# Optimization experiments

Measured on AMD Instinct MI355X. Metric: run time of the kernel, lower is better.

## Reference

```python
import jax, jax.numpy as jnp
import numpy as np

NEMBED, EMBED_DIM, HID_DIM, OUT_DIM, NUM_CLASSES = 128, 64, 128, 128, 2
BATCH, TEAM = 2048, 5
N_OPS = 8


def setup_inputs() -> dict:
    key = jax.random.key(0)
    ks = jax.random.split(key, 8)
    w_eq = np.sqrt(2.0 / (EMBED_DIM + HID_DIM + N_OPS))
    return {
        "x": jax.random.randint(ks[0], (BATCH, 2, TEAM), 0, NEMBED, dtype=jnp.int32),
        "embed": jax.random.normal(ks[1], (NEMBED, EMBED_DIM), jnp.float32) * 0.1,
        "coefs1": jax.random.normal(ks[2], (EMBED_DIM, HID_DIM, N_OPS), jnp.float32) * w_eq,
        "bias1": jnp.zeros((HID_DIM,), jnp.float32),
        "wout1": jax.random.normal(ks[3], (HID_DIM, OUT_DIM), jnp.float32) * np.sqrt(1.0 / HID_DIM),
        "bout1": jnp.zeros((OUT_DIM,), jnp.float32),
        "coefs2": jax.random.normal(ks[4], (EMBED_DIM, HID_DIM, N_OPS), jnp.float32) * w_eq,
        "bias2": jnp.zeros((HID_DIM,), jnp.float32),
        "wout2": jax.random.normal(ks[5], (HID_DIM, OUT_DIM), jnp.float32) * np.sqrt(1.0 / HID_DIM),
        "bout2": jnp.zeros((OUT_DIM,), jnp.float32),
        "fcw": jax.random.normal(ks[6], (2 * OUT_DIM, NCLS := NUM_CLASSES and 2 * OUT_DIM and NUM_CLASSES), jnp.float32) * np.sqrt(1.0 / (2 * OUT_DIM)),
        "fcb": jnp.zeros((NUM_CLASSES,), jnp.float32),
    }


def eset_ops_3_to_3(t):
    # t: (N, D, m, m, m). 8 equivariant basis ops: keep-or-(sum&broadcast) each axis.
    # Pooled ops are kept with singleton dims; broadcasting happens after the
    # channel contraction (cheaper, same math as expand-then-contract).
    s1 = t.sum(-3, keepdims=True)
    s2 = t.sum(-2, keepdims=True)
    s3 = t.sum(-1, keepdims=True)
    s12 = t.sum((-3, -2), keepdims=True)
    s13 = t.sum((-3, -1), keepdims=True)
    s23 = t.sum((-2, -1), keepdims=True)
    sall = t.sum((-3, -2, -1), keepdims=True)
    return [t, s1, s2, s3, s12, s13, s23, sall]


def eq3_layer(t, coefs, bias):
    # coefs: (D_in, D_out, 8); output (N, D_out, m, m, m)
    ops = eset_ops_3_to_3(t)
    out = 0.0
    for b, op in enumerate(ops):
        out = out + jnp.einsum('ndijk,ds->nsijk', op, coefs[:, :, b])
    return out + bias[None, :, None, None, None]


def setnet3to3(t, coefs, bias, wout, bout):
    h = jax.nn.relu(eq3_layer(t, coefs, bias))          # (N, H, m, m, m)
    return jnp.einsum('nsijk,so->nijko', h, wout) + bout  # (N, m, m, m, out_dim)


def reference(x, embed, coefs1, bias1, wout1, bout1, coefs2, bias2, wout2, bout2, fcw, fcb):
    e1 = jax.nn.relu(embed[x[:, 0]])  # (N, 5, D)
    e2 = jax.nn.relu(embed[x[:, 1]])
    t1 = jnp.einsum('bid,bjd,bkd->bdijk', e1, e1, e1)  # (N, D, 5, 5, 5)
    t2 = jnp.einsum('bid,bjd,bkd->bdijk', e2, e2, e2)
    o1 = setnet3to3(t1, coefs1, bias1, wout1, bout1)
    o2 = setnet3to3(t2, coefs2, bias2, wout2, bout2)
    t1e = jax.nn.relu(o1.mean(axis=(1, 2, 3)))  # (N, out_dim)
    t2e = jax.nn.relu(o2.mean(axis=(1, 2, 3)))
    z = jnp.concatenate([t1e, t2e], axis=-1)    # dropout_prob=0 / eval mode: no-op
    return z @ fcw + fcb
```

## Files before the change

### kernel.cpp

```cpp
#include <hip/hip_runtime.h>


typedef __attribute__((ext_vector_type(8))) short bf16x8;
typedef __attribute__((ext_vector_type(4))) float f32x4;
typedef __attribute__((ext_vector_type(4))) unsigned u32x4;

#define DEV __device__ __forceinline__
#define MFMA __builtin_amdgcn_mfma_f32_16x16x32_bf16

DEV constexpr int pid2(int a, int b) {
  int x = a < b ? a : b, y = a < b ? b : a;
  return x * (9 - x) / 2 + y;
}
DEV constexpr int tid3(int i, int j, int k) {
  int a = i, b = j, c = k, t;
  if (a > b) { t = a; a = b; b = t; }
  if (b > c) { t = b; b = c; c = t; }
  if (a > b) { t = a; a = b; b = t; }
  return a * (a * a - 18 * a + 107) / 6 + (b - a) * (11 - a - b) / 2 + (c - b);
}
DEV ushort f2bf(float f) {
  unsigned u = __builtin_bit_cast(unsigned, f);
  return (ushort)((u + 0x7FFFu + ((u >> 16) & 1u)) >> 16);
}
DEV unsigned pk2(float a, float b) {
  return (unsigned)f2bf(a) | ((unsigned)f2bf(b) << 16);
}

__global__ __launch_bounds__(256)
void prep_kernel(const float* __restrict__ c1, const float* __restrict__ c2,
                 const float* __restrict__ w1, const float* __restrict__ w2,
                 ushort* __restrict__ ctf, float* __restrict__ wt, int do_wt) {
  const int idx = blockIdx.x * 256 + threadIdx.x;
  if (idx < 131072) {
    const int e = idx & 7, l = (idx >> 3) & 63, nt = (idx >> 9) & 7,
              kt = (idx >> 12) & 1, bank = (idx >> 13) & 7, side = (idx >> 16) & 1;
    const int d = 32 * kt + 8 * (l >> 4) + e;
    const int s = 16 * nt + (l & 15);
    ctf[idx] = f2bf((side ? c2 : c1)[(d * 128 + s) * 8 + bank]);
  } else if (do_wt) {
    const int j = idx - 131072;
    if (j < 65536) {
      const int s = j & 127, o = (j >> 7) & 127, side = j >> 14;
      wt[j] = (side ? w2 : w1)[s * 128 + o] * (1.f / 125.f);
    }
  }
}

__global__ __launch_bounds__(256, 3)
void eq3_wavegemm(const int* __restrict__ x, const float* __restrict__ embed,
                  const float* __restrict__ bias1, const float* __restrict__ bias2,
                  const float* __restrict__ bout1, const float* __restrict__ bout2,
                  const float* __restrict__ wout1, const float* __restrict__ wout2,
                  const float* __restrict__ fcw,
                  const ushort* __restrict__ ctf, const float* __restrict__ wt,
                  float* __restrict__ pbuf, int nunits)
{
  __shared__ ushort FT[80 * 64];
  __shared__ ushort TS[8 * 2184];
  __shared__ float  S2[256];
  __shared__ float  SW[256];
  __shared__ float  fcp[4];

  const int tid = threadIdx.x;
  const int w = tid >> 6, l = tid & 63, grp = l >> 4, lc = l & 15;

  for (int e = tid; e < 24 * 64; e += 256) {
    const int r = e >> 6, d = e & 63;
    const int row = (r < 13) ? 35 + r : ((r == 13) ? 63 : 70 + (r - 14));
    FT[(row * 64 + d) ^ ((row & 7) << 3)] = 0;
  }
  int uprev = -1;

  for (int u = blockIdx.x; u < nunits; u += gridDim.x) {
    const int side = u & 1;

    {
      const int d = tid & 63, q = tid >> 6;
      const int* xn = x + u * 5;
      float v[5];
      #pragma unroll
      for (int i = 0; i < 5; ++i) v[i] = fmaxf(embed[xn[i] * 64 + d], 0.f);
      const float Sv = v[0] + v[1] + v[2] + v[3] + v[4];
      const float Sq = Sv * Sv, Sc = Sq * Sv;
      float p2a[15];
      {
        int c2 = 0;
        #pragma unroll
        for (int a = 0; a < 5; ++a)
          #pragma unroll
          for (int b = a; b < 5; ++b) { p2a[c2] = v[a] * v[b]; ++c2; }
      }
      {
        int c3 = 0;
        #pragma unroll
        for (int a = 0; a < 5; ++a)
          #pragma unroll
          for (int b = a; b < 5; ++b)
            #pragma unroll
            for (int c = b; c < 5; ++c) {
              const int qq = (c3 < 14) ? 0 : ((c3 < 28) ? 1 : 2);
              if (q == qq)
                FT[(c3 * 64 + d) ^ ((c3 & 7) << 3)] = f2bf(p2a[pid2(a, b)] * v[c]);
              ++c3;
            }
      }
      #pragma unroll
      for (int p = 0; p < 15; ++p) {
        const int qq = (p < 7) ? 2 : 3;
        const int row = 48 + p;
        if (q == qq) FT[(row * 64 + d) ^ ((row & 7) << 3)] = f2bf(Sv * p2a[p]);
      }
      if (q == 3) {
        #pragma unroll
        for (int i = 0; i < 5; ++i) {
          const int row = 64 + i;
          FT[(row * 64 + d) ^ ((row & 7) << 3)] = f2bf(Sq * v[i]);
        }
        FT[(69 * 64 + d) ^ ((69 & 7) << 3)] = f2bf(Sc);
      }
    }
    __syncthreads();

    if (uprev >= 0 && tid == 0) {
      pbuf[2 * uprev]     = fcp[0] + fcp[2];
      pbuf[2 * uprev + 1] = fcp[1] + fcp[3];
    }

    {
      const ushort* cbase = ctf + side * 65536;
      #pragma unroll
      for (int sub = 0; sub < 2; ++sub) {
        const int nti = 2 * w + sub;
        auto FR = [&](int t0, int kt) -> bf16x8 {
          const int t = t0 + lc;
          return *(const bf16x8*)(FT + ((t * 64 + 32 * kt + 8 * grp) ^ ((t & 7) << 3)));
        };
        auto CR = [&](int bank, int kt) -> bf16x8 {
          return *(const bf16x8*)(cbase + (((bank * 2 + kt) * 8 + nti) * 64 + l) * 8);
        };
        ushort* tb = TS + nti * 2184 + lc * 136;
        f32x4 a;
        a = {0.f, 0.f, 0.f, 0.f};
        a = MFMA(FR(0, 0), CR(0, 0), a, 0, 0, 0);
        a = MFMA(FR(0, 1), CR(0, 1), a, 0, 0, 0);
        { uint2 t2; t2.x = pk2(a[0], a[1]); t2.y = pk2(a[2], a[3]);
          *reinterpret_cast<uint2*>(tb + 4 * grp) = t2; }
        a = {0.f, 0.f, 0.f, 0.f};
        a = MFMA(FR(16, 0), CR(0, 0), a, 0, 0, 0);
        a = MFMA(FR(16, 1), CR(0, 1), a, 0, 0, 0);
        { uint2 t2; t2.x = pk2(a[0], a[1]); t2.y = pk2(a[2], a[3]);
          *reinterpret_cast<uint2*>(tb + 16 + 4 * grp) = t2; }
        a = {0.f, 0.f, 0.f, 0.f};
        a = MFMA(FR(32, 0), CR(0, 0), a, 0, 0, 0);
        a = MFMA(FR(32, 1), CR(0, 1), a, 0, 0, 0);
        if (grp == 0) {
          *reinterpret_cast<unsigned*>(tb + 32) = pk2(a[0], a[1]);
          tb[34] = f2bf(a[2]);
        }
        {
          const bf16x8 A0 = FR(48, 0), A1 = FR(48, 1);
          #pragma unroll
          for (int bk = 1; bk <= 3; ++bk) {
            const int cb = 48 + 16 * (bk - 1);
            a = {0.f, 0.f, 0.f, 0.f};
            a = MFMA(A0, CR(bk, 0), a, 0, 0, 0);
            a = MFMA(A1, CR(bk, 1), a, 0, 0, 0);
            if (grp < 3) {
              uint2 t2; t2.x = pk2(a[0], a[1]); t2.y = pk2(a[2], a[3]);
              *reinterpret_cast<uint2*>(tb + cb + 4 * grp) = t2;
            } else {
              *reinterpret_cast<unsigned*>(tb + cb + 12) = pk2(a[0], a[1]);
              tb[cb + 14] = f2bf(a[2]);
            }
          }
        }
        {
          const bf16x8 A0 = FR(64, 0), A1 = FR(64, 1);
          #pragma unroll
          for (int bk = 4; bk <= 6; ++bk) {
            const int cb = 96 + 8 * (bk - 4);
            a = {0.f, 0.f, 0.f, 0.f};
            a = MFMA(A0, CR(bk, 0), a, 0, 0, 0);
            a = MFMA(A1, CR(bk, 1), a, 0, 0, 0);
            if (grp == 0) {
              uint2 t2; t2.x = pk2(a[0], a[1]); t2.y = pk2(a[2], a[3]);
              *reinterpret_cast<uint2*>(tb + cb) = t2;
            } else if (grp == 1) {
              tb[cb + 4] = f2bf(a[0]);
            }
          }
          a = {0.f, 0.f, 0.f, 0.f};
          a = MFMA(A0, CR(7, 0), a, 0, 0, 0);
          a = MFMA(A1, CR(7, 1), a, 0, 0, 0);
          if (grp == 1) tb[120] = f2bf(a[1]);
        }
      }
    }
    __syncthreads();

    {
      const int ch = tid & 127, half = tid >> 7;
      const ushort* trow = TS + (ch >> 4) * 2184 + (ch & 15) * 136;
      u32x4 R[16];
      #pragma unroll
      for (int j = 0; j < 16; ++j) R[j] = *(const u32x4*)(trow + 8 * j);
      __builtin_amdgcn_sched_barrier(0);
      auto ext = [&](int c) -> float {
        const unsigned wv = R[c >> 3][(c >> 1) & 3];
        return __builtin_bit_cast(float, (c & 1) ? (wv & 0xFFFF0000u) : (wv << 16));
      };
      const float* bi = side ? bias2 : bias1;
      const float base = ext(120) + bi[ch];
      float hs = 0.f;
      #define CELLK(i, j, k)                                                      \
        hs += fmaxf(pij + ext(96 + (k)) + ext(64 + pid2(i, k)) +                  \
                    ext(48 + pid2(j, k)) + ext(tid3(i, j, k)), 0.f);
      if (half == 0) {
        #pragma unroll
        for (int i = 0; i < 2; ++i) {
          const float pi = base + ext(112 + i);
          #pragma unroll
          for (int j = 0; j < 5; ++j) {
            const float pij = pi + ext(104 + j) + ext(80 + pid2(i, j));
            #pragma unroll
            for (int k = 0; k < 5; ++k) CELLK(i, j, k)
          }
        }
        {
          const float pi = base + ext(112 + 2);
          #pragma unroll
          for (int j = 0; j < 2; ++j) {
            const float pij = pi + ext(104 + j) + ext(80 + pid2(2, j));
            #pragma unroll
            for (int k = 0; k < 5; ++k) CELLK(2, j, k)
          }
          {
            const float pij = pi + ext(104 + 2) + ext(80 + pid2(2, 2));
            #pragma unroll
            for (int k = 0; k < 3; ++k) CELLK(2, 2, k)
          }
        }
      } else {
        {
          const float pi = base + ext(112 + 2);
          {
            const float pij = pi + ext(104 + 2) + ext(80 + pid2(2, 2));
            #pragma unroll
            for (int k = 3; k < 5; ++k) CELLK(2, 2, k)
          }
          #pragma unroll
          for (int j = 3; j < 5; ++j) {
            const float pij = pi + ext(104 + j) + ext(80 + pid2(2, j));
            #pragma unroll
            for (int k = 0; k < 5; ++k) CELLK(2, j, k)
          }
        }
        #pragma unroll
        for (int i = 3; i < 5; ++i) {
          const float pi = base + ext(112 + i);
          #pragma unroll
          for (int j = 0; j < 5; ++j) {
            const float pij = pi + ext(104 + j) + ext(80 + pid2(i, j));
            #pragma unroll
            for (int k = 0; k < 5; ++k) CELLK(i, j, k)
          }
        }
      }
      #undef CELLK
      S2[half * 128 + ch] = hs;
    }
    __syncthreads();

    {
      const int o = tid & 127, h = tid >> 7;
      float r;
      if (wt != nullptr) {
        const f32x4* wv = (const f32x4*)(wt + side * 16384 + o * 128 + h * 64);
        const f32x4* pa = (const f32x4*)(S2 + h * 64);
        const f32x4* pb = (const f32x4*)(S2 + 128 + h * 64);
        float a0 = 0.f, a1 = 0.f, a2 = 0.f, a3 = 0.f;
        #pragma unroll
        for (int q2 = 0; q2 < 16; ++q2) {
          const f32x4 hq = pa[q2] + pb[q2];
          const f32x4 wq = wv[q2];
          a0 = fmaf(hq[0], wq[0], a0);
          a1 = fmaf(hq[1], wq[1], a1);
          a2 = fmaf(hq[2], wq[2], a2);
          a3 = fmaf(hq[3], wq[3], a3);
        }
        r = (a0 + a1) + (a2 + a3);
      } else {
        const float* W = side ? wout2 : wout1;
        float acc = 0.f;
        #pragma unroll 8
        for (int s = 64 * h; s < 64 * h + 64; ++s)
          acc = fmaf((S2[s] + S2[128 + s]) * (1.f / 125.f), W[s * 128 + o], acc);
        r = acc;
      }
      SW[h * 128 + o] = r;
    }
    __syncthreads();

    if (tid < 128) {
      const int o = tid;
      const float* bo = side ? bout2 : bout1;
      const float z = fmaxf(SW[o] + SW[128 + o] + bo[o], 0.f);
      const float* fw = fcw + side * 256;
      float p0 = z * fw[2 * o], p1 = z * fw[2 * o + 1];
      #pragma unroll
      for (int off = 32; off; off >>= 1) {
        p0 += __shfl_down(p0, off);
        p1 += __shfl_down(p1, off);
      }
      if ((tid & 63) == 0) { fcp[(tid >> 6) * 2] = p0; fcp[(tid >> 6) * 2 + 1] = p1; }
    }
    uprev = u;
  }

  if (uprev >= 0) {
    __syncthreads();
    if (tid == 0) {
      pbuf[2 * uprev]     = fcp[0] + fcp[2];
      pbuf[2 * uprev + 1] = fcp[1] + fcp[3];
    }
  }
}

__global__ __launch_bounds__(256)
void fc_final(const float* __restrict__ pbuf, const float* __restrict__ fcb,
              float* __restrict__ out, int nout) {
  const int t = blockIdx.x * 256 + threadIdx.x;
  if (t < nout) {
    const int n = t >> 1, c = t & 1;
    out[t] = pbuf[4 * n + c] + pbuf[4 * n + 2 + c] + fcb[c];
  }
}

extern "C" void kernel_launch(void* const* d_in, const int* in_sizes, int n_in,
                              void* d_out, int out_size, void* d_ws, size_t ws_size,
                              hipStream_t stream) {
  const int*   x      = (const int*)  d_in[0];
  const float* embed  = (const float*)d_in[1];
  const float* coefs1 = (const float*)d_in[2];
  const float* bias1  = (const float*)d_in[3];
  const float* wout1  = (const float*)d_in[4];
  const float* bout1  = (const float*)d_in[5];
  const float* coefs2 = (const float*)d_in[6];
  const float* bias2  = (const float*)d_in[7];
  const float* wout2  = (const float*)d_in[8];
  const float* bout2  = (const float*)d_in[9];
  const float* fcw    = (const float*)d_in[10];
  const float* fcb    = (const float*)d_in[11];
  float* out = (float*)d_out;

  float*  pbuf = (float*)d_ws;
  ushort* ctf  = (ushort*)((char*)d_ws + 32768);
  const int do_wt = (ws_size >= (size_t)(32768 + 262144 + 131072)) ? 1 : 0;
  float*  wt   = do_wt ? (float*)((char*)d_ws + 32768 + 262144) : nullptr;

  const int batch  = in_sizes[0] / 10;
  const int nunits = batch * 2;

  prep_kernel<<<768, 256, 0, stream>>>(coefs1, coefs2, wout1, wout2, ctf, wt, do_wt);
  eq3_wavegemm<<<2048, 256, 0, stream>>>(
      x, embed, bias1, bias2, bout1, bout2, wout1, wout2, fcw, ctf, wt, pbuf, nunits);
  fc_final<<<(nunits + 255) / 256, 256, 0, stream>>>(pbuf, fcb, out, nunits);
}
```

Before: 92.64 us.

## Use 512-thread blocks with 8 waves, one N-tile per wave

Doubles the block to 8 waves so each wave computes a single MFMA N-tile instead of two, and splits the 125-cell ReLU pass and the output projection four ways across channels instead of two. The grid shrinks from 2048 to 512 persistent blocks, each looping over more units. The aim is shorter per-unit critical paths and more parallel work inside each block. The trade-off is fewer blocks, different occupancy limits and the same number of barriers per unit shared across more threads.

```diff
diff --git a/kernel.cpp b/kernel.cpp
--- a/kernel.cpp
+++ b/kernel.cpp
@@ -47,25 +47,25 @@
   }
 }
 
-__global__ __launch_bounds__(256, 3)
-void eq3_wavegemm(const int* __restrict__ x, const float* __restrict__ embed,
-                  const float* __restrict__ bias1, const float* __restrict__ bias2,
-                  const float* __restrict__ bout1, const float* __restrict__ bout2,
-                  const float* __restrict__ wout1, const float* __restrict__ wout2,
-                  const float* __restrict__ fcw,
-                  const ushort* __restrict__ ctf, const float* __restrict__ wt,
-                  float* __restrict__ pbuf, int nunits)
+__global__ __launch_bounds__(512, 4)
+void eq3_w8(const int* __restrict__ x, const float* __restrict__ embed,
+            const float* __restrict__ bias1, const float* __restrict__ bias2,
+            const float* __restrict__ bout1, const float* __restrict__ bout2,
+            const float* __restrict__ wout1, const float* __restrict__ wout2,
+            const float* __restrict__ fcw,
+            const ushort* __restrict__ ctf, const float* __restrict__ wt,
+            float* __restrict__ pbuf, int nunits)
 {
   __shared__ ushort FT[80 * 64];
   __shared__ ushort TS[8 * 2184];
-  __shared__ float  S2[256];
-  __shared__ float  SW[256];
+  __shared__ float  S2[512];
+  __shared__ float  SW[512];
   __shared__ float  fcp[4];
 
   const int tid = threadIdx.x;
   const int w = tid >> 6, l = tid & 63, grp = l >> 4, lc = l & 15;
 
-  for (int e = tid; e < 24 * 64; e += 256) {
+  for (int e = tid; e < 24 * 64; e += 512) {
     const int r = e >> 6, d = e & 63;
     const int row = (r < 13) ? 35 + r : ((r == 13) ? 63 : 70 + (r - 14));
     FT[(row * 64 + d) ^ ((row & 7) << 3)] = 0;
@@ -99,19 +99,18 @@
           for (int b = a; b < 5; ++b)
             #pragma unroll
             for (int c = b; c < 5; ++c) {
-              const int qq = (c3 < 14) ? 0 : ((c3 < 28) ? 1 : 2);
-              if (q == qq)
+              if (q == c3 / 7)
                 FT[(c3 * 64 + d) ^ ((c3 & 7) << 3)] = f2bf(p2a[pid2(a, b)] * v[c]);
               ++c3;
             }
       }
       #pragma unroll
       for (int p = 0; p < 15; ++p) {
-        const int qq = (p < 7) ? 2 : 3;
         const int row = 48 + p;
-        if (q == qq) FT[(row * 64 + d) ^ ((row & 7) << 3)] = f2bf(Sv * p2a[p]);
-      }
-      if (q == 3) {
+        if (q == (35 + p) / 7)
+          FT[(row * 64 + d) ^ ((row & 7) << 3)] = f2bf(Sv * p2a[p]);
+      }
+      if (q == 7) {
         #pragma unroll
         for (int i = 0; i < 5; ++i) {
           const int row = 64 + i;
@@ -129,78 +128,75 @@
 
     {
       const ushort* cbase = ctf + side * 65536;
-      #pragma unroll
-      for (int sub = 0; sub < 2; ++sub) {
-        const int nti = 2 * w + sub;
-        auto FR = [&](int t0, int kt) -> bf16x8 {
-          const int t = t0 + lc;
-          return *(const bf16x8*)(FT + ((t * 64 + 32 * kt + 8 * grp) ^ ((t & 7) << 3)));
-        };
-        auto CR = [&](int bank, int kt) -> bf16x8 {
-          return *(const bf16x8*)(cbase + (((bank * 2 + kt) * 8 + nti) * 64 + l) * 8);
-        };
-        ushort* tb = TS + nti * 2184 + lc * 136;
-        f32x4 a;
-        a = {0.f, 0.f, 0.f, 0.f};
-        a = MFMA(FR(0, 0), CR(0, 0), a, 0, 0, 0);
-        a = MFMA(FR(0, 1), CR(0, 1), a, 0, 0, 0);
-        { uint2 t2; t2.x = pk2(a[0], a[1]); t2.y = pk2(a[2], a[3]);
-          *reinterpret_cast<uint2*>(tb + 4 * grp) = t2; }
-        a = {0.f, 0.f, 0.f, 0.f};
-        a = MFMA(FR(16, 0), CR(0, 0), a, 0, 0, 0);
-        a = MFMA(FR(16, 1), CR(0, 1), a, 0, 0, 0);
-        { uint2 t2; t2.x = pk2(a[0], a[1]); t2.y = pk2(a[2], a[3]);
-          *reinterpret_cast<uint2*>(tb + 16 + 4 * grp) = t2; }
-        a = {0.f, 0.f, 0.f, 0.f};
-        a = MFMA(FR(32, 0), CR(0, 0), a, 0, 0, 0);
-        a = MFMA(FR(32, 1), CR(0, 1), a, 0, 0, 0);
-        if (grp == 0) {
-          *reinterpret_cast<unsigned*>(tb + 32) = pk2(a[0], a[1]);
-          tb[34] = f2bf(a[2]);
-        }
-        {
-          const bf16x8 A0 = FR(48, 0), A1 = FR(48, 1);
-          #pragma unroll
-          for (int bk = 1; bk <= 3; ++bk) {
-            const int cb = 48 + 16 * (bk - 1);
-            a = {0.f, 0.f, 0.f, 0.f};
-            a = MFMA(A0, CR(bk, 0), a, 0, 0, 0);
-            a = MFMA(A1, CR(bk, 1), a, 0, 0, 0);
-            if (grp < 3) {
-              uint2 t2; t2.x = pk2(a[0], a[1]); t2.y = pk2(a[2], a[3]);
-              *reinterpret_cast<uint2*>(tb + cb + 4 * grp) = t2;
-            } else {
-              *reinterpret_cast<unsigned*>(tb + cb + 12) = pk2(a[0], a[1]);
-              tb[cb + 14] = f2bf(a[2]);
-            }
+      const int nti = w;
+      auto FR = [&](int t0, int kt) -> bf16x8 {
+        const int t = t0 + lc;
+        return *(const bf16x8*)(FT + ((t * 64 + 32 * kt + 8 * grp) ^ ((t & 7) << 3)));
+      };
+      auto CR = [&](int bank, int kt) -> bf16x8 {
+        return *(const bf16x8*)(cbase + (((bank * 2 + kt) * 8 + nti) * 64 + l) * 8);
+      };
+      ushort* tb = TS + nti * 2184 + lc * 136;
+      f32x4 a;
+      a = {0.f, 0.f, 0.f, 0.f};
+      a = MFMA(FR(0, 0), CR(0, 0), a, 0, 0, 0);
+      a = MFMA(FR(0, 1), CR(0, 1), a, 0, 0, 0);
+      { uint2 t2; t2.x = pk2(a[0], a[1]); t2.y = pk2(a[2], a[3]);
+        *reinterpret_cast<uint2*>(tb + 4 * grp) = t2; }
+      a = {0.f, 0.f, 0.f, 0.f};
+      a = MFMA(FR(16, 0), CR(0, 0), a, 0, 0, 0);
+      a = MFMA(FR(16, 1), CR(0, 1), a, 0, 0, 0);
+      { uint2 t2; t2.x = pk2(a[0], a[1]); t2.y = pk2(a[2], a[3]);
+        *reinterpret_cast<uint2*>(tb + 16 + 4 * grp) = t2; }
+      a = {0.f, 0.f, 0.f, 0.f};
+      a = MFMA(FR(32, 0), CR(0, 0), a, 0, 0, 0);
+      a = MFMA(FR(32, 1), CR(0, 1), a, 0, 0, 0);
+      if (grp == 0) {
+        *reinterpret_cast<unsigned*>(tb + 32) = pk2(a[0], a[1]);
+        tb[34] = f2bf(a[2]);
+      }
+      {
+        const bf16x8 A0 = FR(48, 0), A1 = FR(48, 1);
+        #pragma unroll
+        for (int bk = 1; bk <= 3; ++bk) {
+          const int cb = 48 + 16 * (bk - 1);
+          a = {0.f, 0.f, 0.f, 0.f};
+          a = MFMA(A0, CR(bk, 0), a, 0, 0, 0);
+          a = MFMA(A1, CR(bk, 1), a, 0, 0, 0);
+          if (grp < 3) {
+            uint2 t2; t2.x = pk2(a[0], a[1]); t2.y = pk2(a[2], a[3]);
+            *reinterpret_cast<uint2*>(tb + cb + 4 * grp) = t2;
+          } else {
+            *reinterpret_cast<unsigned*>(tb + cb + 12) = pk2(a[0], a[1]);
+            tb[cb + 14] = f2bf(a[2]);
           }
         }
-        {
-          const bf16x8 A0 = FR(64, 0), A1 = FR(64, 1);
-          #pragma unroll
-          for (int bk = 4; bk <= 6; ++bk) {
-            const int cb = 96 + 8 * (bk - 4);
-            a = {0.f, 0.f, 0.f, 0.f};
-            a = MFMA(A0, CR(bk, 0), a, 0, 0, 0);
-            a = MFMA(A1, CR(bk, 1), a, 0, 0, 0);
-            if (grp == 0) {
-              uint2 t2; t2.x = pk2(a[0], a[1]); t2.y = pk2(a[2], a[3]);
-              *reinterpret_cast<uint2*>(tb + cb) = t2;
-            } else if (grp == 1) {
-              tb[cb + 4] = f2bf(a[0]);
-            }
+      }
+      {
+        const bf16x8 A0 = FR(64, 0), A1 = FR(64, 1);
+        #pragma unroll
+        for (int bk = 4; bk <= 6; ++bk) {
+          const int cb = 96 + 8 * (bk - 4);
+          a = {0.f, 0.f, 0.f, 0.f};
+          a = MFMA(A0, CR(bk, 0), a, 0, 0, 0);
+          a = MFMA(A1, CR(bk, 1), a, 0, 0, 0);
+          if (grp == 0) {
+            uint2 t2; t2.x = pk2(a[0], a[1]); t2.y = pk2(a[2], a[3]);
+            *reinterpret_cast<uint2*>(tb + cb) = t2;
+          } else if (grp == 1) {
+            tb[cb + 4] = f2bf(a[0]);
           }
-          a = {0.f, 0.f, 0.f, 0.f};
-          a = MFMA(A0, CR(7, 0), a, 0, 0, 0);
-          a = MFMA(A1, CR(7, 1), a, 0, 0, 0);
-          if (grp == 1) tb[120] = f2bf(a[1]);
         }
+        a = {0.f, 0.f, 0.f, 0.f};
+        a = MFMA(A0, CR(7, 0), a, 0, 0, 0);
+        a = MFMA(A1, CR(7, 1), a, 0, 0, 0);
+        if (grp == 1) tb[120] = f2bf(a[1]);
       }
     }
     __syncthreads();
 
     {
-      const int ch = tid & 127, half = tid >> 7;
+      const int ch = tid & 127, cq = tid >> 7;
       const ushort* trow = TS + (ch >> 4) * 2184 + (ch & 15) * 136;
       u32x4 R[16];
       #pragma unroll
@@ -213,76 +209,43 @@
       const float* bi = side ? bias2 : bias1;
       const float base = ext(120) + bi[ch];
       float hs = 0.f;
-      #define CELLK(i, j, k)                                                      \
-        hs += fmaxf(pij + ext(96 + (k)) + ext(64 + pid2(i, k)) +                  \
-                    ext(48 + pid2(j, k)) + ext(tid3(i, j, k)), 0.f);
-      if (half == 0) {
-        #pragma unroll
-        for (int i = 0; i < 2; ++i) {
-          const float pi = base + ext(112 + i);
-          #pragma unroll
-          for (int j = 0; j < 5; ++j) {
-            const float pij = pi + ext(104 + j) + ext(80 + pid2(i, j));
-            #pragma unroll
-            for (int k = 0; k < 5; ++k) CELLK(i, j, k)
-          }
-        }
-        {
-          const float pi = base + ext(112 + 2);
-          #pragma unroll
-          for (int j = 0; j < 2; ++j) {
-            const float pij = pi + ext(104 + j) + ext(80 + pid2(2, j));
-            #pragma unroll
-            for (int k = 0; k < 5; ++k) CELLK(2, j, k)
-          }
-          {
-            const float pij = pi + ext(104 + 2) + ext(80 + pid2(2, 2));
-            #pragma unroll
-            for (int k = 0; k < 3; ++k) CELLK(2, 2, k)
-          }
-        }
+      auto cellf = [&](int c) {
+        const int i = c / 25, j = (c / 5) % 5, k = c % 5;
+        const float val = base + ext(112 + i) + ext(104 + j) + ext(80 + pid2(i, j))
+                        + ext(96 + k) + ext(64 + pid2(i, k)) + ext(48 + pid2(j, k))
+                        + ext(tid3(i, j, k));
+        hs += fmaxf(val, 0.f);
+      };
+      if (cq == 0) {
+        #pragma unroll
+        for (int c = 0; c < 31; ++c) cellf(c);
+      } else if (cq == 1) {
+        #pragma unroll
+        for (int c = 31; c < 62; ++c) cellf(c);
+      } else if (cq == 2) {
+        #pragma unroll
+        for (int c = 62; c < 93; ++c) cellf(c);
       } else {
-        {
-          const float pi = base + ext(112 + 2);
-          {
-            const float pij = pi + ext(104 + 2) + ext(80 + pid2(2, 2));
-            #pragma unroll
-            for (int k = 3; k < 5; ++k) CELLK(2, 2, k)
-          }
-          #pragma unroll
-          for (int j = 3; j < 5; ++j) {
-            const float pij = pi + ext(104 + j) + ext(80 + pid2(2, j));
-            #pragma unroll
-            for (int k = 0; k < 5; ++k) CELLK(2, j, k)
-          }
-        }
-        #pragma unroll
-        for (int i = 3; i < 5; ++i) {
-          const float pi = base + ext(112 + i);
-          #pragma unroll
-          for (int j = 0; j < 5; ++j) {
-            const float pij = pi + ext(104 + j) + ext(80 + pid2(i, j));
-            #pragma unroll
-            for (int k = 0; k < 5; ++k) CELLK(i, j, k)
-          }
-        }
-      }
-      #undef CELLK
-      S2[half * 128 + ch] = hs;
+        #pragma unroll
+        for (int c = 93; c < 125; ++c) cellf(c);
+      }
+      S2[cq * 128 + ch] = hs;
     }
     __syncthreads();
 
     {
-      const int o = tid & 127, h = tid >> 7;
+      const int o = tid & 127, sq = tid >> 7;
       float r;
       if (wt != nullptr) {
-        const f32x4* wv = (const f32x4*)(wt + side * 16384 + o * 128 + h * 64);
-        const f32x4* pa = (const f32x4*)(S2 + h * 64);
-        const f32x4* pb = (const f32x4*)(S2 + 128 + h * 64);
+        const f32x4* wv = (const f32x4*)(wt + side * 16384 + o * 128 + sq * 32);
+        const f32x4* pa = (const f32x4*)(S2 + sq * 32);
+        const f32x4* pb = (const f32x4*)(S2 + 128 + sq * 32);
+        const f32x4* pc = (const f32x4*)(S2 + 256 + sq * 32);
+        const f32x4* pd = (const f32x4*)(S2 + 384 + sq * 32);
         float a0 = 0.f, a1 = 0.f, a2 = 0.f, a3 = 0.f;
         #pragma unroll
-        for (int q2 = 0; q2 < 16; ++q2) {
-          const f32x4 hq = pa[q2] + pb[q2];
+        for (int q2 = 0; q2 < 8; ++q2) {
+          const f32x4 hq = (pa[q2] + pb[q2]) + (pc[q2] + pd[q2]);
           const f32x4 wq = wv[q2];
           a0 = fmaf(hq[0], wq[0], a0);
           a1 = fmaf(hq[1], wq[1], a1);
@@ -294,18 +257,19 @@
         const float* W = side ? wout2 : wout1;
         float acc = 0.f;
         #pragma unroll 8
-        for (int s = 64 * h; s < 64 * h + 64; ++s)
-          acc = fmaf((S2[s] + S2[128 + s]) * (1.f / 125.f), W[s * 128 + o], acc);
+        for (int s = 32 * sq; s < 32 * sq + 32; ++s)
+          acc = fmaf((S2[s] + S2[128 + s] + S2[256 + s] + S2[384 + s]) * (1.f / 125.f),
+                     W[s * 128 + o], acc);
         r = acc;
       }
-      SW[h * 128 + o] = r;
+      SW[sq * 128 + o] = r;
     }
     __syncthreads();
 
     if (tid < 128) {
       const int o = tid;
       const float* bo = side ? bout2 : bout1;
-      const float z = fmaxf(SW[o] + SW[128 + o] + bo[o], 0.f);
+      const float z = fmaxf(SW[o] + SW[128 + o] + SW[256 + o] + SW[384 + o] + bo[o], 0.f);
       const float* fw = fcw + side * 256;
       float p0 = z * fw[2 * o], p1 = z * fw[2 * o + 1];
       #pragma unroll
@@ -363,7 +327,7 @@
   const int nunits = batch * 2;
 
   prep_kernel<<<768, 256, 0, stream>>>(coefs1, coefs2, wout1, wout2, ctf, wt, do_wt);
-  eq3_wavegemm<<<2048, 256, 0, stream>>>(
+  eq3_w8<<<512, 512, 0, stream>>>(
       x, embed, bias1, bias2, bout1, bout2, wout1, wout2, fcw, ctf, wt, pbuf, nunits);
   fc_final<<<(nunits + 255) / 256, 256, 0, stream>>>(pbuf, fcb, out, nunits);
 }
```

After: 95.32 us. 1.03x slower.
